# Optimization experiments

Hardware: AMD Instinct MI355X
Metric: run time of the kernel (lower is better)

The kernel has to match this reference:

```python
import jax, jax.numpy as jnp
import numpy as np

B, S, D = 2, 2048, 2048
H, KVH = 16, 4
HD = D // H          # 128 head dim
KVD = KVH * HD       # 512
BASE = 10000.0
EPS = 1.1920929e-07  # float32 eps, matches torch F.rms_norm default


def setup_inputs() -> dict:
    key = jax.random.key(0)
    ks = jax.random.split(key, 9)
    sd = 1.0 / np.sqrt(D)
    x = jax.random.normal(ks[0], (B, S, D), jnp.float32)
    Wq = jax.random.normal(ks[1], (D, D), jnp.float32) * sd
    bq = jnp.zeros((D,), jnp.float32)
    Wk = jax.random.normal(ks[2], (KVD, D), jnp.float32) * sd
    bk = jnp.zeros((KVD,), jnp.float32)
    Wv = jax.random.normal(ks[3], (KVD, D), jnp.float32) * sd
    bv = jnp.zeros((KVD,), jnp.float32)
    Wo = jax.random.normal(ks[4], (D, D), jnp.float32) * sd
    bo = jnp.zeros((D,), jnp.float32)
    q_gain = jnp.ones((H,), jnp.float32)
    return {"x": x, "Wq": Wq, "bq": bq, "Wk": Wk, "bk": bk,
            "Wv": Wv, "bv": bv, "Wo": Wo, "bo": bo, "q_gain": q_gain}


def _rms_norm(t):
    return t * jax.lax.rsqrt(jnp.mean(t * t, axis=-1, keepdims=True) + EPS)


def _rope_tables(s, dtype):
    inv_freq = 1.0 / (BASE ** (jnp.arange(0, HD, 2, dtype=jnp.float32) / HD))  # [HD/2]
    t = jnp.arange(s, dtype=jnp.float32)
    freqs = jnp.outer(t, inv_freq)                       # [s, HD/2]
    cos = jnp.cos(freqs)[None, None].astype(dtype)       # [1,1,s,HD/2]
    sin = jnp.sin(freqs)[None, None].astype(dtype)
    return cos, sin


def _apply_rope(t, cos, sin):
    half = t.shape[-1] // 2
    t1, t2 = t[..., :half], t[..., half:]
    return jnp.concatenate([t1 * cos + t2 * sin, -t1 * sin + t2 * cos], axis=-1)


def reference(x, Wq, bq, Wk, bk, Wv, bv, Wo, bo, q_gain):
    b, s, d = x.shape
    q = (jnp.einsum('bsd,ed->bse', x, Wq) + bq).reshape(b, s, H, HD).transpose(0, 2, 1, 3)
    k = (jnp.einsum('bsd,ed->bse', x, Wk) + bk).reshape(b, s, KVH, HD).transpose(0, 2, 1, 3)
    v = (jnp.einsum('bsd,ed->bse', x, Wv) + bv).reshape(b, s, KVH, HD).transpose(0, 2, 1, 3)
    # QK RMSNorm (no learned weight)
    q = _rms_norm(q)
    k = _rms_norm(k)
    # RoPE over full head dim (rope_dims=0 path)
    cos, sin = _rope_tables(s, q.dtype)
    q = _apply_rope(q, cos, sin)
    k = _apply_rope(k, cos, sin)
    # per-head gain on q
    q = q * q_gain[None, :, None, None]
    # GQA: repeat kv heads
    rep = H // KVH
    k = jnp.repeat(k, rep, axis=1)
    v = jnp.repeat(v, rep, axis=1)
    scale = HD ** -0.5
    attn = jnp.einsum('bhqd,bhkd->bhqk', q * scale, k)   # [b,H,s,s]
    causal = jnp.tril(jnp.ones((s, s), dtype=bool))
    attn = jnp.where(causal[None, None], attn, -jnp.inf)
    attn = jax.nn.softmax(attn, axis=-1)
    out = jnp.einsum('bhqk,bhkd->bqhd', attn, v).reshape(b, s, d)
    return jnp.einsum('bsd,ed->bse', out, Wo) + bo
```

## Files before the change

### kernel.cpp

```cpp
#include <hip/hip_runtime.h>
#include <hip/hip_bf16.h>

typedef __hip_bfloat16 bf16;
typedef unsigned short u16;
typedef short short8 __attribute__((ext_vector_type(8)));
typedef float f32x4  __attribute__((ext_vector_type(4)));

static __device__ __forceinline__ float b2f(u16 u) {
    union { unsigned int i; float f; } c; c.i = (unsigned int)u << 16; return c.f;
}

static __device__ __forceinline__ float ldf(const void* p, size_t i, int isbf16) {
    return isbf16 ? __bfloat162float(((const bf16*)p)[i]) : ((const float*)p)[i];
}
static __device__ __forceinline__ void stf(void* p, size_t i, float v, int isbf16) {
    if (isbf16) ((bf16*)p)[i] = __float2bfloat16(v);
    else        ((float*)p)[i] = v;
}

static __device__ __forceinline__ unsigned packf(float v) {
    unsigned ub = __float_as_uint(v);
    unsigned uh = ub & 0xFFFF0000u;
    float r = v - __uint_as_float(uh);
    return uh | (__float_as_uint(r) >> 16);
}
static __device__ __forceinline__ float unpackf(unsigned u) {
    return __uint_as_float(u & 0xFFFF0000u) + __uint_as_float(u << 16);
}

static __device__ __forceinline__ void upk8(uint4 a, uint4 b, short8& h, short8& l) {
    h = (short8){(short)(a.x >> 16), (short)(a.y >> 16), (short)(a.z >> 16), (short)(a.w >> 16),
                 (short)(b.x >> 16), (short)(b.y >> 16), (short)(b.z >> 16), (short)(b.w >> 16)};
    l = (short8){(short)(a.x), (short)(a.y), (short)(a.z), (short)(a.w),
                 (short)(b.x), (short)(b.y), (short)(b.z), (short)(b.w)};
}

static __device__ __forceinline__ void splitf8(float4 a, float4 b, short8& h, short8& l) {
    float vv[8] = {a.x, a.y, a.z, a.w, b.x, b.y, b.z, b.w};
    unsigned hh[8], ll[8];
#pragma unroll
    for (int j = 0; j < 8; j++) {
        unsigned ub = __float_as_uint(vv[j]);
        unsigned uh = ub & 0xFFFF0000u;
        float r = vv[j] - __uint_as_float(uh);
        hh[j] = uh >> 16;
        ll[j] = __float_as_uint(r) >> 16;
    }
    h = (short8){(short)hh[0], (short)hh[1], (short)hh[2], (short)hh[3],
                 (short)hh[4], (short)hh[5], (short)hh[6], (short)hh[7]};
    l = (short8){(short)ll[0], (short)ll[1], (short)ll[2], (short)ll[3],
                 (short)ll[4], (short)ll[5], (short)ll[6], (short)ll[7]};
}

static __device__ __forceinline__ float4 u2f4(uint4 a) {
    return (float4){__uint_as_float(a.x), __uint_as_float(a.y),
                    __uint_as_float(a.z), __uint_as_float(a.w)};
}
static __device__ __forceinline__ short8 u4_s8(uint4 a) {
    return (short8){(short)(a.x & 0xFFFF), (short)(a.x >> 16),
                    (short)(a.y & 0xFFFF), (short)(a.y >> 16),
                    (short)(a.z & 0xFFFF), (short)(a.z >> 16),
                    (short)(a.w & 0xFFFF), (short)(a.w >> 16)};
}

template<int MODE>
static __device__ __forceinline__ void load_any(const void* P, size_t e, int f, uint4* r) {
    if (MODE == 2) {
        const uint4* p = (const uint4*)((const unsigned*)P + e);
        r[0] = p[0]; r[1] = p[1]; r[2] = p[2]; r[3] = p[3];
    } else if (f == 0) {
        const uint4* p = (const uint4*)((const float*)P + e);
        r[0] = p[0]; r[1] = p[1]; r[2] = p[2]; r[3] = p[3];
    } else {
        const uint4* p = (const uint4*)((const u16*)P + e);
        r[0] = p[0]; r[1] = p[1];
        r[2] = (uint4){0, 0, 0, 0}; r[3] = (uint4){0, 0, 0, 0};
    }
}
template<int MODE>
static __device__ __forceinline__ void conv_any(const uint4* r, int f,
        short8& h0, short8& h1, short8& l0, short8& l1) {
    if (MODE == 2) {
        upk8(r[0], r[1], h0, l0);
        upk8(r[2], r[3], h1, l1);
    } else if (f == 0) {
        splitf8(u2f4(r[0]), u2f4(r[1]), h0, l0);
        splitf8(u2f4(r[2]), u2f4(r[3]), h1, l1);
    } else {
        h0 = u4_s8(r[0]); h1 = u4_s8(r[1]);
        l0 = (short8){0,0,0,0,0,0,0,0};
        l1 = (short8){0,0,0,0,0,0,0,0};
    }
}

static __device__ __forceinline__ void async_copy16(const void* g, void* l) {
    __builtin_amdgcn_global_load_lds((const __attribute__((address_space(1))) void*)g,
                                     (__attribute__((address_space(3))) void*)l, 16, 0, 0);
}

__global__ void detect_dtype(const unsigned short* __restrict__ x, int n, int* __restrict__ flag)
{
    __shared__ int cnt;
    if (threadIdx.x == 0) cnt = 0;
    __syncthreads();
    int local = 0;
    for (int i = threadIdx.x; i < n; i += blockDim.x) {
        const unsigned int e = (x[i] >> 7) & 0xFF;
        if (e >= 134u) local++;
    }
    atomicAdd(&cnt, local);
    __syncthreads();
    if (threadIdx.x == 0) *flag = (cnt >= 32) ? 0 : 1;
}

__global__ __launch_bounds__(256)
void split_x(const void* __restrict__ x, u16* __restrict__ Xh, u16* __restrict__ Xl,
             const int* __restrict__ flagp)
{
    const int f = *flagp;
    const size_t i = ((size_t)blockIdx.x * 256 + threadIdx.x) * 8;
    if (f == 0) {
        const float4* p = (const float4*)((const float*)x + i);
        short8 h, l;
        splitf8(p[0], p[1], h, l);
        *(short8*)(Xh + i) = h;
        *(short8*)(Xl + i) = l;
    } else {
        *(short8*)(Xh + i) = *(const short8*)((const u16*)x + i);
        *(short8*)(Xl + i) = (short8){0,0,0,0,0,0,0,0};
    }
}

template<int AM, int BM, int OUT, int BROW>
static __device__ __forceinline__ void gemm_core(
    const void* __restrict__ Aa, const void* __restrict__ Ab,
    const void* __restrict__ Ba, const void* __restrict__ Bb,
    const void* __restrict__ bias, void* __restrict__ Ca,
    int N, int K, int f, int bx, int by, u16* sm)
{
    u16* AhT = sm;
    u16* AlT = sm + 4096;
    u16* WhT = sm + 8192;
    u16* WlT = sm + 12288;

    const int t = threadIdx.x;
    const int w = t >> 6, lane = t & 63;
    const int wm = w >> 1, wn = w & 1;
    const int lr = lane & 15, quad = lane >> 4;
    const int bm = by * 128, bn = bx * 128;
    const int arow = lane >> 2;
    const int acol = (lane & 3) * 8;
    const int srow = t >> 1, scol = (t & 1) * 16;

    f32x4 acc[4][4];
#pragma unroll
    for (int i = 0; i < 4; i++)
#pragma unroll
        for (int j = 0; j < 4; j++) acc[i][j] = (f32x4){0.f, 0.f, 0.f, 0.f};

    uint4 ra[4], rb[4];
    const size_t aBase = (size_t)(bm + srow) * K + scol;
    const size_t bBase = (size_t)(bn + srow) * K + scol;
    if (AM != 1) load_any<AM>(Aa, aBase, f, ra);
    if (BM != 1) load_any<BM>(Ba, bBase, f, rb);

    for (int k0 = 0; k0 < K; k0 += 32) {
        __syncthreads();
        if (AM == 1) {
#pragma unroll
            for (int c = 2 * w; c < 2 * w + 2; c++) {
                const int row = c * 16 + arow;
                async_copy16((const u16*)Aa + (size_t)(bm + row) * K + k0 + acol, &AhT[c * 512]);
                async_copy16((const u16*)Ab + (size_t)(bm + row) * K + k0 + acol, &AlT[c * 512]);
            }
        } else {
            short8 h0, h1, l0, l1;
            conv_any<AM>(ra, f, h0, h1, l0, l1);
            const int o = srow * 32 + scol;
            *(short8*)&AhT[o] = h0; *(short8*)&AhT[o + 8] = h1;
            *(short8*)&AlT[o] = l0; *(short8*)&AlT[o + 8] = l1;
        }
        if (BM == 1) {
#pragma unroll
            for (int c = 2 * w; c < 2 * w + 2; c++) {
                const int row = c * 16 + arow;
                async_copy16((const u16*)Ba + (size_t)(bn + row) * K + k0 + acol, &WhT[c * 512]);
                async_copy16((const u16*)Bb + (size_t)(bn + row) * K + k0 + acol, &WlT[c * 512]);
            }
        } else {
            short8 h0, h1, l0, l1;
            conv_any<BM>(rb, f, h0, h1, l0, l1);
            const int o = srow * 32 + scol;
            *(short8*)&WhT[o] = h0; *(short8*)&WhT[o + 8] = h1;
            *(short8*)&WlT[o] = l0; *(short8*)&WlT[o + 8] = l1;
        }
        __syncthreads();
        if (k0 + 32 < K) {
            if (AM != 1) load_any<AM>(Aa, aBase + k0 + 32, f, ra);
            if (BM != 1) load_any<BM>(Ba, bBase + k0 + 32, f, rb);
        }

        short8 avh[4], avl[4], bvh[4], bvl[4];
#pragma unroll
        for (int i = 0; i < 4; i++) {
            const int o = (wm * 64 + i * 16 + lr) * 32 + quad * 8;
            avh[i] = *(const short8*)&AhT[o];
            avl[i] = *(const short8*)&AlT[o];
        }
#pragma unroll
        for (int j = 0; j < 4; j++) {
            const int o = (wn * 64 + j * 16 + lr) * 32 + quad * 8;
            bvh[j] = *(const short8*)&WhT[o];
            bvl[j] = *(const short8*)&WlT[o];
        }
        __builtin_amdgcn_s_setprio(1);
#pragma unroll
        for (int i = 0; i < 4; i++)
#pragma unroll
            for (int j = 0; j < 4; j++)
                acc[i][j] = __builtin_amdgcn_mfma_f32_16x16x32_bf16(avl[i], bvh[j], acc[i][j], 0, 0, 0);
#pragma unroll
        for (int i = 0; i < 4; i++)
#pragma unroll
            for (int j = 0; j < 4; j++)
                acc[i][j] = __builtin_amdgcn_mfma_f32_16x16x32_bf16(avh[i], bvl[j], acc[i][j], 0, 0, 0);
#pragma unroll
        for (int i = 0; i < 4; i++)
#pragma unroll
            for (int j = 0; j < 4; j++)
                acc[i][j] = __builtin_amdgcn_mfma_f32_16x16x32_bf16(avh[i], bvh[j], acc[i][j], 0, 0, 0);
        __builtin_amdgcn_s_setprio(0);
    }

#pragma unroll
    for (int j = 0; j < 4; j++) {
        const int col = bn + wn * 64 + j * 16 + lr;
        const float bc = BROW ? 0.f : ldf(bias, col, f);
#pragma unroll
        for (int i = 0; i < 4; i++) {
            const int row0 = bm + wm * 64 + i * 16 + quad * 4;
#pragma unroll
            for (int r = 0; r < 4; r++) {
                const int row = row0 + r;
                const float bb = BROW ? ldf(bias, row, f) : bc;
                const float val = acc[i][j][r] + bb;
                const size_t idx = (size_t)row * N + col;
                if (OUT == 1) ((unsigned*)Ca)[idx] = packf(val);
                else          stf(Ca, idx, val, f);
            }
        }
    }
}

__global__ __launch_bounds__(256, 3)
void gemm_qkv(const u16* __restrict__ Xh, const u16* __restrict__ Xl,
              const void* __restrict__ Wq, const void* __restrict__ bq, unsigned* __restrict__ Qp,
              const void* __restrict__ Wk, const void* __restrict__ bk, unsigned* __restrict__ Kp,
              const void* __restrict__ Wv, const void* __restrict__ bv, unsigned* __restrict__ Vtp,
              const int* __restrict__ flagp)
{
    __shared__ __align__(16) u16 sm[16384];
    const int f = *flagp;
    const int id = blockIdx.x;
    if (id < 512) {
        gemm_core<1, 0, 1, 0>(Xh, Xl, Wq, nullptr, bq, Qp,
                              2048, 2048, f, id & 15, id >> 4, sm);
    } else if (id < 640) {
        const int v = id - 512;
        gemm_core<1, 0, 1, 0>(Xh, Xl, Wk, nullptr, bk, Kp,
                              512, 2048, f, v & 3, v >> 2, sm);
    } else {
        const int v = id - 640;
        gemm_core<0, 1, 1, 1>(Wv, nullptr, Xh, Xl, bv, Vtp,
                              4096, 2048, f, v >> 2, v & 3, sm);
    }
}

__global__ __launch_bounds__(256, 3)
void gemm_o(const u16* __restrict__ Ch, const u16* __restrict__ Cl,
            const void* __restrict__ Wo, const void* __restrict__ bo,
            void* __restrict__ out, const int* __restrict__ flagp)
{
    __shared__ __align__(16) u16 sm[16384];
    gemm_core<1, 0, 2, 0>(Ch, Cl, Wo, nullptr, bo, out,
                          2048, 2048, *flagp, blockIdx.x & 15, blockIdx.x >> 4, sm);
}

__global__ __launch_bounds__(64)
void norm_rope_pk(unsigned* __restrict__ buf, const void* __restrict__ gain,
                  int nheads, float scale, const int* __restrict__ flagp)
{
    const int id = blockIdx.x;
    const int h  = id % nheads;
    const int bs = id / nheads;
    const int s  = bs & 2047;
    unsigned* v = buf + (size_t)bs * nheads * 128 + h * 128;
    const int i = threadIdx.x;

    float t1 = unpackf(v[i]);
    float t2 = unpackf(v[i + 64]);
    float ss = t1 * t1 + t2 * t2;
#pragma unroll
    for (int off = 32; off >= 1; off >>= 1) ss += __shfl_xor(ss, off);
    const float r = rsqrtf(ss * (1.0f / 128.0f) + 1.1920929e-07f);
    t1 *= r; t2 *= r;

    const float inv_freq = exp2f(-(float)i * 0.20762050593046014f);
    const float ph = (float)s * inv_freq;
    float sn, cs;
    __sincosf(ph, &sn, &cs);

    float g = scale;
    if (gain) g *= ldf(gain, h, *flagp);

    v[i]      = packf((t1 * cs + t2 * sn) * g);
    v[i + 64] = packf((-t1 * sn + t2 * cs) * g);
}

__global__ __launch_bounds__(256, 2)
void attn3(const unsigned* __restrict__ Qp, const unsigned* __restrict__ Kp,
           const unsigned* __restrict__ Vtp,
           u16* __restrict__ Chg, u16* __restrict__ Clg)
{
    const int S = 2048, D = 2048, KVD = 512, MT = 4096;

    __shared__ __align__(16) u16 Kh[64 * 128], Kl[64 * 128];
    __shared__ __align__(16) u16 Vh[128 * 64], Vl[128 * 64];
    __shared__ __align__(16) u16 Ps[4][16][72];

    const int t = threadIdx.x, w = t >> 6, lane = t & 63;
    const int lr = lane & 15, quad = lane >> 4;
    const int h = blockIdx.y, b = blockIdx.z;
    const int kvh = h >> 2;

    const int qt0 = blockIdx.x;
    const int qt1 = 31 - blockIdx.x;
    const int nt0 = qt0 + 1, nt1 = qt1 + 1;
    const int total = nt0 + nt1;

    const int kr = t >> 2, kq = t & 3;
    const int vd = t >> 1, vh2 = t & 1;
    const unsigned* kg = Kp + (size_t)(b * S + kr) * KVD + kvh * 128 + kq * 32;
    const unsigned* vg = Vtp + (size_t)(kvh * 128 + vd) * MT + b * S + vh2 * 32;
    char* KhB = (char*)Kh; char* KlB = (char*)Kl;
    char* VhB = (char*)Vh; char* VlB = (char*)Vl;

    uint4 kv[8], vv[8];
#define ISSUE_KV(K0)                                                     \
    do {                                                                 \
        _Pragma("unroll")                                                \
        for (int u = 0; u < 8; u++) {                                    \
            kv[u] = *(const uint4*)(kg + (size_t)(K0) * KVD + u * 4);    \
            vv[u] = *(const uint4*)(vg + (K0) + u * 4);                  \
        }                                                                \
    } while (0)

    short8 qh[4], ql[4];
    f32x4 acc[8];
    float mreg[4], lreg[4];
    int q0 = 0, nt = nt0;

    ISSUE_KV(0);

    for (int it = 0; it < total; it++) {
        const int item = (it >= nt0) ? 1 : 0;
        const int kt = item ? (it - nt0) : it;
        if (kt == 0) {
            nt = item ? nt1 : nt0;
            q0 = (item ? qt1 : qt0) * 64;
            const unsigned* qs = Qp + (size_t)(b * S + q0 + w * 16 + lr) * D + h * 128;
#pragma unroll
            for (int kk = 0; kk < 4; kk++) {
                const uint4* p = (const uint4*)(qs + kk * 32 + quad * 8);
                upk8(p[0], p[1], qh[kk], ql[kk]);
            }
#pragma unroll
            for (int dt = 0; dt < 8; dt++) acc[dt] = (f32x4){0.f, 0.f, 0.f, 0.f};
#pragma unroll
            for (int r = 0; r < 4; r++) { mreg[r] = -1e30f; lreg[r] = 0.f; }
        }
        const int k0 = kt * 64;

        __syncthreads();
#pragma unroll
        for (int u2 = 0; u2 < 4; u2++) {
            short8 hh, ll;
            upk8(kv[2 * u2], kv[2 * u2 + 1], hh, ll);
            const int ko = (kr * 256 + kq * 64 + u2 * 16) ^ ((kr & 7) << 4);
            *(short8*)(KhB + ko) = hh;
            *(short8*)(KlB + ko) = ll;
            upk8(vv[2 * u2], vv[2 * u2 + 1], hh, ll);
            const int vo = (vd * 128 + vh2 * 64 + u2 * 16) ^ ((vd & 7) << 4);
            *(short8*)(VhB + vo) = hh;
            *(short8*)(VlB + vo) = ll;
        }
        __syncthreads();

        if (it + 1 < total) {
            const int nk0 = (it + 1 >= nt0) ? (it + 1 - nt0) * 64 : (it + 1) * 64;
            ISSUE_KV(nk0);
        }

        f32x4 sacc[4];
#pragma unroll
        for (int ct = 0; ct < 4; ct++) sacc[ct] = (f32x4){0.f, 0.f, 0.f, 0.f};
#pragma unroll
        for (int ks = 0; ks < 4; ks++) {
            short8 kbh[4], kbl[4];
#pragma unroll
            for (int ct = 0; ct < 4; ct++) {
                const int row = ct * 16 + lr;
                const int off = (row * 256 + ks * 64 + quad * 16) ^ ((row & 7) << 4);
                kbh[ct] = *(const short8*)(KhB + off);
                kbl[ct] = *(const short8*)(KlB + off);
            }
            __builtin_amdgcn_s_setprio(1);
#pragma unroll
            for (int ct = 0; ct < 4; ct++)
                sacc[ct] = __builtin_amdgcn_mfma_f32_16x16x32_bf16(ql[ks], kbh[ct], sacc[ct], 0, 0, 0);
#pragma unroll
            for (int ct = 0; ct < 4; ct++)
                sacc[ct] = __builtin_amdgcn_mfma_f32_16x16x32_bf16(qh[ks], kbl[ct], sacc[ct], 0, 0, 0);
#pragma unroll
            for (int ct = 0; ct < 4; ct++)
                sacc[ct] = __builtin_amdgcn_mfma_f32_16x16x32_bf16(qh[ks], kbh[ct], sacc[ct], 0, 0, 0);
            __builtin_amdgcn_s_setprio(0);
        }

        const bool diag = (kt == nt - 1);
        float p[4][4];
#pragma unroll
        for (int r = 0; r < 4; r++) {
            const int qg = q0 + w * 16 + quad * 4 + r;
            float s0 = sacc[0][r], s1 = sacc[1][r], s2 = sacc[2][r], s3 = sacc[3][r];
            if (diag) {
                if (k0 +  0 + lr > qg) s0 = -1e30f;
                if (k0 + 16 + lr > qg) s1 = -1e30f;
                if (k0 + 32 + lr > qg) s2 = -1e30f;
                if (k0 + 48 + lr > qg) s3 = -1e30f;
            }
            float mt = fmaxf(fmaxf(s0, s1), fmaxf(s2, s3));
#pragma unroll
            for (int off = 1; off < 16; off <<= 1) mt = fmaxf(mt, __shfl_xor(mt, off));
            const float mnew  = fmaxf(mreg[r], mt);
            const float alpha = __expf(mreg[r] - mnew);
            p[r][0] = (s0 <= -1e29f) ? 0.f : __expf(s0 - mnew);
            p[r][1] = (s1 <= -1e29f) ? 0.f : __expf(s1 - mnew);
            p[r][2] = (s2 <= -1e29f) ? 0.f : __expf(s2 - mnew);
            p[r][3] = (s3 <= -1e29f) ? 0.f : __expf(s3 - mnew);
            float ps = p[r][0] + p[r][1] + p[r][2] + p[r][3];
#pragma unroll
            for (int off = 1; off < 16; off <<= 1) ps += __shfl_xor(ps, off);
            lreg[r] = lreg[r] * alpha + ps;
            mreg[r] = mnew;
#pragma unroll
            for (int dt = 0; dt < 8; dt++) acc[dt][r] *= alpha;
        }

#pragma unroll
        for (int r = 0; r < 4; r++)
#pragma unroll
            for (int ct = 0; ct < 4; ct++)
                Ps[w][quad * 4 + r][ct * 16 + lr] = (u16)(__float_as_uint(p[r][ct]) >> 16);
#pragma unroll
        for (int ks2 = 0; ks2 < 2; ks2++) {
            const short8 pa = *(const short8*)((const char*)&Ps[w][lr][0] + ks2 * 64 + quad * 16);
            __builtin_amdgcn_s_setprio(1);
#pragma unroll
            for (int dt = 0; dt < 8; dt++) {
                const int vrow = dt * 16 + lr;
                const int off = (vrow * 128 + ks2 * 64 + quad * 16) ^ ((vrow & 7) << 4);
                const short8 vbh = *(const short8*)(VhB + off);
                acc[dt] = __builtin_amdgcn_mfma_f32_16x16x32_bf16(pa, vbh, acc[dt], 0, 0, 0);
            }
#pragma unroll
            for (int dt = 0; dt < 8; dt++) {
                const int vrow = dt * 16 + lr;
                const int off = (vrow * 128 + ks2 * 64 + quad * 16) ^ ((vrow & 7) << 4);
                const short8 vbl = *(const short8*)(VlB + off);
                acc[dt] = __builtin_amdgcn_mfma_f32_16x16x32_bf16(pa, vbl, acc[dt], 0, 0, 0);
            }
            __builtin_amdgcn_s_setprio(0);
        }
#pragma unroll
        for (int r = 0; r < 4; r++)
#pragma unroll
            for (int ct = 0; ct < 4; ct++) {
                const unsigned ub = __float_as_uint(p[r][ct]);
                const unsigned uh = ub & 0xFFFF0000u;
                const float rr = p[r][ct] - __uint_as_float(uh);
                Ps[w][quad * 4 + r][ct * 16 + lr] = (u16)(__float_as_uint(rr) >> 16);
            }
#pragma unroll
        for (int ks2 = 0; ks2 < 2; ks2++) {
            const short8 pa = *(const short8*)((const char*)&Ps[w][lr][0] + ks2 * 64 + quad * 16);
            __builtin_amdgcn_s_setprio(1);
#pragma unroll
            for (int dt = 0; dt < 8; dt++) {
                const int vrow = dt * 16 + lr;
                const int off = (vrow * 128 + ks2 * 64 + quad * 16) ^ ((vrow & 7) << 4);
                const short8 vbh = *(const short8*)(VhB + off);
                acc[dt] = __builtin_amdgcn_mfma_f32_16x16x32_bf16(pa, vbh, acc[dt], 0, 0, 0);
            }
            __builtin_amdgcn_s_setprio(0);
        }

        if (kt == nt - 1) {
#pragma unroll
            for (int r = 0; r < 4; r++) {
                const float inv = 1.0f / lreg[r];
                const size_t base = (size_t)(b * S + q0 + w * 16 + quad * 4 + r) * D + h * 128 + lr;
#pragma unroll
                for (int dt = 0; dt < 8; dt++) {
                    const float val = acc[dt][r] * inv;
                    const unsigned ub = __float_as_uint(val);
                    const unsigned uh = ub & 0xFFFF0000u;
                    Chg[base + dt * 16] = (u16)(uh >> 16);
                    Clg[base + dt * 16] = (u16)(__float_as_uint(val - __uint_as_float(uh)) >> 16);
                }
            }
        }
    }
#undef ISSUE_KV
}

extern "C" void kernel_launch(void* const* d_in, const int* in_sizes, int n_in,
                              void* d_out, int out_size, void* d_ws, size_t ws_size,
                              hipStream_t stream)
{
    const void* x  = d_in[0];
    const void* Wq = d_in[1];
    const void* bq = d_in[2];
    const void* Wk = d_in[3];
    const void* bk = d_in[4];
    const void* Wv = d_in[5];
    const void* bv = d_in[6];
    const void* Wo = d_in[7];
    const void* bo = d_in[8];
    const void* qg = d_in[9];

    const int B = 2, S = 2048, D = 2048, H = 16, KVH = 4, KVD = 512;
    const int M = B * S;

    unsigned* Qp  = (unsigned*)d_ws;
    unsigned* Kp  = Qp + (size_t)M * D;
    unsigned* Vtp = Kp + (size_t)M * KVD;
    unsigned* Cp  = Vtp + (size_t)KVD * M;
    int* flag = (int*)(Cp + (size_t)M * D);
    u16* CXh = (u16*)Cp;
    u16* CXl = CXh + (size_t)M * D;

    detect_dtype<<<1, 256, 0, stream>>>((const unsigned short*)x, 16384, flag);

    split_x<<<(M * D) / (256 * 8), 256, 0, stream>>>(x, CXh, CXl, flag);

    gemm_qkv<<<768, 256, 0, stream>>>(CXh, CXl, Wq, bq, Qp,
                                      Wk, bk, Kp, Wv, bv, Vtp, flag);

    norm_rope_pk<<<M * H, 64, 0, stream>>>(Qp, qg, H, 0.08838834764831845f, flag);
    norm_rope_pk<<<M * KVH, 64, 0, stream>>>(Kp, nullptr, KVH, 1.0f, flag);

    attn3<<<dim3(16, H, B), 256, 0, stream>>>(Qp, Kp, Vtp, CXh, CXl);

    gemm_o<<<512, 256, 0, stream>>>(CXh, CXl, Wo, bo, d_out, flag);
}
```

Baseline: 659.8 us.

## Store K/V as interleaved hi/lo bf16 blocks, skip unpacking in attention

The K and V projection epilogues now write hi and lo bf16 halves interleaved in 8-element blocks instead of packed 32-bit words. The attention kernel can then copy loaded vectors straight into shared memory without per-tile unpacking, and a new norm/RoPE kernel works on this layout. The online softmax also skips the rescale exponent and accumulator multiply when the row max does not change, and the three-pass QK and two-pass PV MFMA loops are interleaved. The cost is scattered 16-bit stores in the GEMM epilogue and a divergent branch in the softmax.

```diff
diff --git a/kernel.cpp b/kernel.cpp
--- a/kernel.cpp
+++ b/kernel.cpp
@@ -244,9 +244,19 @@
                 const int row = row0 + r;
                 const float bb = BROW ? ldf(bias, row, f) : bc;
                 const float val = acc[i][j][r] + bb;
-                const size_t idx = (size_t)row * N + col;
-                if (OUT == 1) ((unsigned*)Ca)[idx] = packf(val);
-                else          stf(Ca, idx, val, f);
+                if (OUT == 1) {
+                    ((unsigned*)Ca)[(size_t)row * N + col] = packf(val);
+                } else if (OUT == 2) {
+                    stf(Ca, (size_t)row * N + col, val, f);
+                } else {
+                    u16* C16 = (u16*)Ca;
+                    const size_t ii = (size_t)row * ((size_t)N * 2)
+                                    + ((size_t)(col >> 3) << 4) + (col & 7);
+                    const unsigned ub = __float_as_uint(val);
+                    const unsigned uh = ub & 0xFFFF0000u;
+                    C16[ii]     = (u16)(uh >> 16);
+                    C16[ii + 8] = (u16)(__float_as_uint(val - __uint_as_float(uh)) >> 16);
+                }
             }
         }
     }
@@ -255,8 +265,8 @@
 __global__ __launch_bounds__(256, 3)
 void gemm_qkv(const u16* __restrict__ Xh, const u16* __restrict__ Xl,
               const void* __restrict__ Wq, const void* __restrict__ bq, unsigned* __restrict__ Qp,
-              const void* __restrict__ Wk, const void* __restrict__ bk, unsigned* __restrict__ Kp,
-              const void* __restrict__ Wv, const void* __restrict__ bv, unsigned* __restrict__ Vtp,
+              const void* __restrict__ Wk, const void* __restrict__ bk, u16* __restrict__ Kil,
+              const void* __restrict__ Wv, const void* __restrict__ bv, u16* __restrict__ Vtil,
               const int* __restrict__ flagp)
 {
     __shared__ __align__(16) u16 sm[16384];
@@ -267,11 +277,11 @@
                               2048, 2048, f, id & 15, id >> 4, sm);
     } else if (id < 640) {
         const int v = id - 512;
-        gemm_core<1, 0, 1, 0>(Xh, Xl, Wk, nullptr, bk, Kp,
+        gemm_core<1, 0, 4, 0>(Xh, Xl, Wk, nullptr, bk, Kil,
                               512, 2048, f, v & 3, v >> 2, sm);
     } else {
         const int v = id - 640;
-        gemm_core<0, 1, 1, 1>(Wv, nullptr, Xh, Xl, bv, Vtp,
+        gemm_core<0, 1, 4, 1>(Wv, nullptr, Xh, Xl, bv, Vtil,
                               4096, 2048, f, v >> 2, v & 3, sm);
     }
 }
@@ -317,12 +327,51 @@
     v[i + 64] = packf((-t1 * sn + t2 * cs) * g);
 }
 
+__global__ __launch_bounds__(64)
+void norm_rope_il(u16* __restrict__ buf, int nheads)
+{
+    const int id = blockIdx.x;
+    const int h  = id % nheads;
+    const int bs = id / nheads;
+    const int s  = bs & 2047;
+    u16* v = buf + (size_t)bs * (size_t)(nheads * 256);
+    const int i = threadIdx.x;
+    const int c1 = h * 128 + i;
+    const int c2 = c1 + 64;
+    const int a1 = ((c1 >> 3) << 4) + (c1 & 7);
+    const int a2 = ((c2 >> 3) << 4) + (c2 & 7);
+
+    float t1 = b2f(v[a1]) + b2f(v[a1 + 8]);
+    float t2 = b2f(v[a2]) + b2f(v[a2 + 8]);
+    float ss = t1 * t1 + t2 * t2;
+#pragma unroll
+    for (int off = 32; off >= 1; off >>= 1) ss += __shfl_xor(ss, off);
+    const float r = rsqrtf(ss * (1.0f / 128.0f) + 1.1920929e-07f);
+    t1 *= r; t2 *= r;
+
+    const float inv_freq = exp2f(-(float)i * 0.20762050593046014f);
+    const float ph = (float)s * inv_freq;
+    float sn, cs;
+    __sincosf(ph, &sn, &cs);
+
+    const float o1 = t1 * cs + t2 * sn;
+    const float o2 = -t1 * sn + t2 * cs;
+    const unsigned u1 = __float_as_uint(o1) & 0xFFFF0000u;
+    const unsigned u2 = __float_as_uint(o2) & 0xFFFF0000u;
+    v[a1]     = (u16)(u1 >> 16);
+    v[a1 + 8] = (u16)(__float_as_uint(o1 - __uint_as_float(u1)) >> 16);
+    v[a2]     = (u16)(u2 >> 16);
+    v[a2 + 8] = (u16)(__float_as_uint(o2 - __uint_as_float(u2)) >> 16);
+}
+
 __global__ __launch_bounds__(256, 2)
-void attn3(const unsigned* __restrict__ Qp, const unsigned* __restrict__ Kp,
-           const unsigned* __restrict__ Vtp,
+void attn3(const unsigned* __restrict__ Qp, const u16* __restrict__ Kil,
+           const u16* __restrict__ Vtil,
            u16* __restrict__ Chg, u16* __restrict__ Clg)
 {
-    const int S = 2048, D = 2048, KVD = 512, MT = 4096;
+    const int S = 2048, D = 2048;
+    const int KVD2 = 1024;
+    const int MT2  = 8192;
 
     __shared__ __align__(16) u16 Kh[64 * 128], Kl[64 * 128];
     __shared__ __align__(16) u16 Vh[128 * 64], Vl[128 * 64];
@@ -340,19 +389,19 @@
 
     const int kr = t >> 2, kq = t & 3;
     const int vd = t >> 1, vh2 = t & 1;
-    const unsigned* kg = Kp + (size_t)(b * S + kr) * KVD + kvh * 128 + kq * 32;
-    const unsigned* vg = Vtp + (size_t)(kvh * 128 + vd) * MT + b * S + vh2 * 32;
+    const u16* kg = Kil + (size_t)(b * S + kr) * KVD2 + kvh * 256 + kq * 64;
+    const u16* vg = Vtil + (size_t)(kvh * 128 + vd) * MT2 + (size_t)(b * S) * 2 + vh2 * 64;
     char* KhB = (char*)Kh; char* KlB = (char*)Kl;
     char* VhB = (char*)Vh; char* VlB = (char*)Vl;
 
     uint4 kv[8], vv[8];
-#define ISSUE_KV(K0)                                                     \
-    do {                                                                 \
-        _Pragma("unroll")                                                \
-        for (int u = 0; u < 8; u++) {                                    \
-            kv[u] = *(const uint4*)(kg + (size_t)(K0) * KVD + u * 4);    \
-            vv[u] = *(const uint4*)(vg + (K0) + u * 4);                  \
-        }                                                                \
+#define ISSUE_KV(K0)                                                          \
+    do {                                                                      \
+        _Pragma("unroll")                                                     \
+        for (int u = 0; u < 8; u++) {                                         \
+            kv[u] = *(const uint4*)(kg + (size_t)(K0) * KVD2 + u * 8);        \
+            vv[u] = *(const uint4*)(vg + (size_t)(K0) * 2 + u * 8);           \
+        }                                                                     \
     } while (0)
 
     short8 qh[4], ql[4];
@@ -384,15 +433,12 @@
         __syncthreads();
 #pragma unroll
         for (int u2 = 0; u2 < 4; u2++) {
-            short8 hh, ll;
-            upk8(kv[2 * u2], kv[2 * u2 + 1], hh, ll);
             const int ko = (kr * 256 + kq * 64 + u2 * 16) ^ ((kr & 7) << 4);
-            *(short8*)(KhB + ko) = hh;
-            *(short8*)(KlB + ko) = ll;
-            upk8(vv[2 * u2], vv[2 * u2 + 1], hh, ll);
+            *(uint4*)(KhB + ko) = kv[2 * u2];
+            *(uint4*)(KlB + ko) = kv[2 * u2 + 1];
             const int vo = (vd * 128 + vh2 * 64 + u2 * 16) ^ ((vd & 7) << 4);
-            *(short8*)(VhB + vo) = hh;
-            *(short8*)(VlB + vo) = ll;
+            *(uint4*)(VhB + vo) = vv[2 * u2];
+            *(uint4*)(VlB + vo) = vv[2 * u2 + 1];
         }
         __syncthreads();
 
@@ -416,14 +462,11 @@
             }
             __builtin_amdgcn_s_setprio(1);
 #pragma unroll
-            for (int ct = 0; ct < 4; ct++)
+            for (int ct = 0; ct < 4; ct++) {
                 sacc[ct] = __builtin_amdgcn_mfma_f32_16x16x32_bf16(ql[ks], kbh[ct], sacc[ct], 0, 0, 0);
-#pragma unroll
-            for (int ct = 0; ct < 4; ct++)
                 sacc[ct] = __builtin_amdgcn_mfma_f32_16x16x32_bf16(qh[ks], kbl[ct], sacc[ct], 0, 0, 0);
-#pragma unroll
-            for (int ct = 0; ct < 4; ct++)
                 sacc[ct] = __builtin_amdgcn_mfma_f32_16x16x32_bf16(qh[ks], kbh[ct], sacc[ct], 0, 0, 0);
+            }
             __builtin_amdgcn_s_setprio(0);
         }
 
@@ -443,7 +486,6 @@
 #pragma unroll
             for (int off = 1; off < 16; off <<= 1) mt = fmaxf(mt, __shfl_xor(mt, off));
             const float mnew  = fmaxf(mreg[r], mt);
-            const float alpha = __expf(mreg[r] - mnew);
             p[r][0] = (s0 <= -1e29f) ? 0.f : __expf(s0 - mnew);
             p[r][1] = (s1 <= -1e29f) ? 0.f : __expf(s1 - mnew);
             p[r][2] = (s2 <= -1e29f) ? 0.f : __expf(s2 - mnew);
@@ -451,10 +493,15 @@
             float ps = p[r][0] + p[r][1] + p[r][2] + p[r][3];
 #pragma unroll
             for (int off = 1; off < 16; off <<= 1) ps += __shfl_xor(ps, off);
-            lreg[r] = lreg[r] * alpha + ps;
-            mreg[r] = mnew;
-#pragma unroll
-            for (int dt = 0; dt < 8; dt++) acc[dt][r] *= alpha;
+            if (mnew > mreg[r]) {
+                const float alpha = __expf(mreg[r] - mnew);
+                lreg[r] = lreg[r] * alpha + ps;
+                mreg[r] = mnew;
+#pragma unroll
+                for (int dt = 0; dt < 8; dt++) acc[dt][r] *= alpha;
+            } else {
+                lreg[r] += ps;
+            }
         }
 
 #pragma unroll
@@ -471,13 +518,8 @@
                 const int vrow = dt * 16 + lr;
                 const int off = (vrow * 128 + ks2 * 64 + quad * 16) ^ ((vrow & 7) << 4);
                 const short8 vbh = *(const short8*)(VhB + off);
+                const short8 vbl = *(const short8*)(VlB + off);
                 acc[dt] = __builtin_amdgcn_mfma_f32_16x16x32_bf16(pa, vbh, acc[dt], 0, 0, 0);
-            }
-#pragma unroll
-            for (int dt = 0; dt < 8; dt++) {
-                const int vrow = dt * 16 + lr;
-                const int off = (vrow * 128 + ks2 * 64 + quad * 16) ^ ((vrow & 7) << 4);
-                const short8 vbl = *(const short8*)(VlB + off);
                 acc[dt] = __builtin_amdgcn_mfma_f32_16x16x32_bf16(pa, vbl, acc[dt], 0, 0, 0);
             }
             __builtin_amdgcn_s_setprio(0);
@@ -543,24 +585,23 @@
     const int M = B * S;
 
     unsigned* Qp  = (unsigned*)d_ws;
-    unsigned* Kp  = Qp + (size_t)M * D;
-    unsigned* Vtp = Kp + (size_t)M * KVD;
-    unsigned* Cp  = Vtp + (size_t)KVD * M;
-    int* flag = (int*)(Cp + (size_t)M * D);
-    u16* CXh = (u16*)Cp;
-    u16* CXl = CXh + (size_t)M * D;
+    u16* Kil  = (u16*)(Qp + (size_t)M * D);
+    u16* Vtil = Kil + (size_t)M * KVD * 2;
+    u16* CXh  = Vtil + (size_t)KVD * M * 2;
+    u16* CXl  = CXh + (size_t)M * D;
+    int* flag = (int*)(CXl + (size_t)M * D);
 
     detect_dtype<<<1, 256, 0, stream>>>((const unsigned short*)x, 16384, flag);
 
     split_x<<<(M * D) / (256 * 8), 256, 0, stream>>>(x, CXh, CXl, flag);
 
     gemm_qkv<<<768, 256, 0, stream>>>(CXh, CXl, Wq, bq, Qp,
-                                      Wk, bk, Kp, Wv, bv, Vtp, flag);
+                                      Wk, bk, Kil, Wv, bv, Vtil, flag);
 
     norm_rope_pk<<<M * H, 64, 0, stream>>>(Qp, qg, H, 0.08838834764831845f, flag);
-    norm_rope_pk<<<M * KVH, 64, 0, stream>>>(Kp, nullptr, KVH, 1.0f, flag);
-
-    attn3<<<dim3(16, H, B), 256, 0, stream>>>(Qp, Kp, Vtp, CXh, CXl);
+    norm_rope_il<<<M * KVH, 64, 0, stream>>>(Kil, KVH);
+
+    attn3<<<dim3(16, H, B), 256, 0, stream>>>(Qp, Kil, Vtil, CXh, CXl);
 
     gemm_o<<<512, 256, 0, stream>>>(CXh, CXl, Wo, bo, d_out, flag);
 }
```

After: 927.6 us. 1.41x slower.
